# Optimization experiments

Measured on AMD Instinct MI355X. Metric: run time of the kernel, lower is better.

Reference implementation:

```python
import jax, jax.numpy as jnp
from jax import lax
import numpy as np

VOCAB, EMB = 50000, 50
B, S = 256, 2048
K1, K2 = 8, 4  # k-max pool sizes (k1=8 hardcoded, top_k=4)


def conv1d_valid(x, w, b):
    # x: [B, L, Cin], w: [KW, Cin, Cout] (TF conv1d layout), VALID padding
    return lax.conv_general_dilated(
        x, w, window_strides=(1,), padding='VALID',
        dimension_numbers=('NWC', 'WIO', 'NWC')) + b


def kmax_pool(signal, k):
    # Dynamic k-max pooling: select k positions with largest channel-mean
    # excitement (tf.nn.top_k sorted=False + gather over axis 1).
    excitements = jnp.mean(signal, axis=2)            # [B, L]
    _, idx = lax.top_k(excitements, k)                # [B, k]
    return jnp.take_along_axis(signal, idx[:, :, None], axis=1)  # [B, k, C]


def setup_inputs() -> dict:
    key = jax.random.key(0)
    ks = jax.random.split(key, 6)
    x = jax.random.randint(ks[0], (B, S), 0, VOCAB, dtype=jnp.int32)
    embeddings = jax.random.normal(ks[1], (VOCAB, EMB), jnp.float32)
    W1 = jax.random.normal(ks[2], (7, EMB, 6), jnp.float32) * 0.05
    b1 = jnp.zeros((6,), jnp.float32)
    W2 = jax.random.normal(ks[3], (5, 6, 14), jnp.float32) * 0.1
    b2 = jnp.zeros((14,), jnp.float32)
    Wd = jax.random.normal(ks[4], (14, 1), jnp.float32) * 0.1
    bd = jnp.zeros((1,), jnp.float32)
    return {"x": x, "embeddings": embeddings, "W1": W1, "b1": b1,
            "W2": W2, "b2": b2, "Wd": Wd, "bd": bd}


def reference(x, embeddings, W1, b1, W2, b2, Wd, bd):
    signal = embeddings[x]                                  # [B, S, 50]
    signal = jnp.pad(signal, ((0, 0), (6, 6), (0, 0)))      # [B, S+12, 50]
    signal = conv1d_valid(signal, W1, b1)                   # [B, S+6, 6]
    signal = kmax_pool(signal, K1)                          # [B, 8, 6]
    signal = jax.nn.sigmoid(signal)
    signal = jnp.pad(signal, ((0, 0), (4, 4), (0, 0)))      # [B, 16, 6]
    signal = conv1d_valid(signal, W2, b2)                   # [B, 12, 14]
    signal = kmax_pool(signal, K2)                          # [B, 4, 14]
    signal = jnp.mean(signal, axis=1)                       # [B, 14]
    dense = signal @ Wd + bd                                # [B, 1]
    output = jnp.mean(dense)                                # scalar
    return jax.nn.sigmoid(output)
```

## Files before the change

kernel.cpp:

```cpp
#include <hip/hip_runtime.h>
#include <math.h>

#define SEQ   2048
#define VOCAB 50000
#define EMBD  50
#define L1OUT 2054
#define NTOK  2060
#define DSTR  2064

__global__ void __launch_bounds__(384)
prep_kernel(const float* __restrict__ W1, float* __restrict__ ws) {
    int t = threadIdx.x;
    if (t < 350) {
        float s = 0.f;
        #pragma unroll
        for (int c = 0; c < 6; ++c) s += W1[t * 6 + c];
        ws[t] = s * (1.0f / 6.0f);
    } else if (t < 352) {
        ws[t] = 0.f;
    }
}

__global__ void __launch_bounds__(256)
build_d(const float* __restrict__ emb, const float* __restrict__ wm,
        float* __restrict__ D) {
    int v = blockIdx.x * 256 + threadIdx.x;
    if (v >= VOCAB) return;
    const float2* row = (const float2*)(emb + (size_t)v * EMBD);
    float d[7] = {0.f, 0.f, 0.f, 0.f, 0.f, 0.f, 0.f};
    for (int e = 0; e < 25; ++e) {
        float2 r = row[e];
        #pragma unroll
        for (int kw = 0; kw < 7; ++kw)
            d[kw] = fmaf(r.y, wm[kw * 50 + 2 * e + 1],
                    fmaf(r.x, wm[kw * 50 + 2 * e], d[kw]));
    }
    float4* out = (float4*)(D + (size_t)v * 8);
    out[0] = make_float4(d[0], d[1], d[2], d[3]);
    out[1] = make_float4(d[4], d[5], d[6], 0.f);
}

template<int USE_D>
__global__ void __launch_bounds__(512, 1)
dcnn_main(const int* __restrict__ x, const float* __restrict__ emb,
          const float* __restrict__ W1, const float* __restrict__ b1,
          const float* __restrict__ W2, const float* __restrict__ b2,
          const float* __restrict__ Wd, const float* __restrict__ bd,
          const float* __restrict__ Dtab, const float* __restrict__ wm,
          float* __restrict__ dense_out)
{
    __shared__ float Dv[7][DSTR];
    __shared__ float exc[L1OUT];
    __shared__ float blv[8];
    __shared__ int   bli[8];
    __shared__ int   topi[8];
    __shared__ float part[240];
    __shared__ float s1p[16][6];
    __shared__ float out2[12][14];
    __shared__ float exc2[12];

    const int b   = blockIdx.x;
    const int tid = threadIdx.x;
    const int* xb = x + b * SEQ;

    for (int i = tid; i < NTOK; i += 512) {
        int g = i - 6;
        float d0 = 0.f, d1 = 0.f, d2 = 0.f, d3 = 0.f,
              d4 = 0.f, d5 = 0.f, d6 = 0.f;
        if (g >= 0 && g < SEQ) {
            int tok = xb[g];
            if (USE_D) {
                const float4* dp = (const float4*)(Dtab + (size_t)tok * 8);
                float4 lo = dp[0], hi = dp[1];
                d0 = lo.x; d1 = lo.y; d2 = lo.z; d3 = lo.w;
                d4 = hi.x; d5 = hi.y; d6 = hi.z;
            } else {
                const float2* row = (const float2*)(emb + (size_t)tok * EMBD);
                float dd[7] = {0.f, 0.f, 0.f, 0.f, 0.f, 0.f, 0.f};
                for (int e = 0; e < 25; ++e) {
                    float2 r = row[e];
                    #pragma unroll
                    for (int kw = 0; kw < 7; ++kw)
                        dd[kw] = fmaf(r.y, wm[kw * 50 + 2 * e + 1],
                                 fmaf(r.x, wm[kw * 50 + 2 * e], dd[kw]));
                }
                d0 = dd[0]; d1 = dd[1]; d2 = dd[2]; d3 = dd[3];
                d4 = dd[4]; d5 = dd[5]; d6 = dd[6];
            }
        }
        Dv[0][i] = d0; Dv[1][i] = d1; Dv[2][i] = d2; Dv[3][i] = d3;
        Dv[4][i] = d4; Dv[5][i] = d5; Dv[6][i] = d6;
    }
    __syncthreads();

    for (int t = tid; t < L1OUT; t += 512) {
        float s = ((Dv[0][t] + Dv[1][t + 1]) + (Dv[2][t + 2] + Dv[3][t + 3]))
                + ((Dv[4][t + 4] + Dv[5][t + 5]) + Dv[6][t + 6]);
        exc[t] = s;
    }
    __syncthreads();

    #pragma unroll 1
    for (int r = 0; r < 8; ++r) {
        float bv = -INFINITY; int bi = L1OUT;
        for (int t = tid; t < L1OUT; t += 512) {
            float v = exc[t];
            if (v > bv || (v == bv && t < bi)) { bv = v; bi = t; }
        }
        #pragma unroll
        for (int off = 32; off > 0; off >>= 1) {
            float ov = __shfl_down(bv, off, 64);
            int   oi = __shfl_down(bi, off, 64);
            if (ov > bv || (ov == bv && oi < bi)) { bv = ov; bi = oi; }
        }
        if ((tid & 63) == 0) { blv[tid >> 6] = bv; bli[tid >> 6] = bi; }
        __syncthreads();
        if (tid == 0) {
            #pragma unroll
            for (int w = 1; w < 8; ++w) {
                float ov = blv[w]; int oi = bli[w];
                if (ov > bv || (ov == bv && oi < bi)) { bv = ov; bi = oi; }
            }
            topi[r] = bi;
            exc[bi] = -INFINITY;
        }
        __syncthreads();
    }

    if (tid < 96) ((float*)s1p)[tid] = 0.f;
    if (tid < 240) {
        int r = tid / 30, sub = tid - r * 30;
        int c = sub / 5,  eq  = sub - c * 5;
        int t = topi[r];
        float acc = 0.f;
        for (int kw = 0; kw < 7; ++kw) {
            int g = t + kw - 6;
            if (g >= 0 && g < SEQ) {
                const float* row = emb + (size_t)xb[g] * EMBD + eq * 10;
                const float* wp  = W1 + (kw * 50 + eq * 10) * 6 + c;
                #pragma unroll
                for (int e = 0; e < 10; ++e)
                    acc = fmaf(row[e], wp[e * 6], acc);
            }
        }
        part[tid] = acc;
    }
    __syncthreads();
    if (tid < 48) {
        int r = tid / 6, c = tid - r * 6;
        float s = b1[c];
        #pragma unroll
        for (int eq = 0; eq < 5; ++eq) s += part[r * 30 + c * 5 + eq];
        s1p[4 + r][c] = 1.0f / (1.0f + expf(-s));
    }
    __syncthreads();

    if (tid < 168) {
        int t = tid / 14, c = tid - t * 14;
        float acc = b2[c];
        #pragma unroll
        for (int kw = 0; kw < 5; ++kw)
            #pragma unroll
            for (int i = 0; i < 6; ++i)
                acc = fmaf(s1p[t + kw][i], W2[(kw * 6 + i) * 14 + c], acc);
        out2[t][c] = acc;
    }
    __syncthreads();
    if (tid < 12) {
        float s = 0.f;
        #pragma unroll
        for (int c = 0; c < 14; ++c) s += out2[tid][c];
        exc2[tid] = s / 14.0f;
    }
    __syncthreads();

    if (tid == 0) {
        float ev[12];
        #pragma unroll
        for (int t = 0; t < 12; ++t) ev[t] = exc2[t];
        int sel[4];
        #pragma unroll 1
        for (int r = 0; r < 4; ++r) {
            float bv = -INFINITY; int bi = 0;
            for (int t = 0; t < 12; ++t)
                if (ev[t] > bv) { bv = ev[t]; bi = t; }
            sel[r] = bi; ev[bi] = -INFINITY;
        }
        float dense = bd[0];
        #pragma unroll
        for (int c = 0; c < 14; ++c) {
            float pool = 0.25f * ((out2[sel[0]][c] + out2[sel[1]][c]) +
                                  (out2[sel[2]][c] + out2[sel[3]][c]));
            dense = fmaf(pool, Wd[c], dense);
        }
        dense_out[b] = dense;
    }
}

__global__ void __launch_bounds__(256)
finalize_kernel(const float* __restrict__ dense, float* __restrict__ out) {
    int tid = threadIdx.x;
    float v = dense[tid];
    #pragma unroll
    for (int off = 32; off > 0; off >>= 1) v += __shfl_down(v, off, 64);
    __shared__ float ws4[4];
    if ((tid & 63) == 0) ws4[tid >> 6] = v;
    __syncthreads();
    if (tid == 0) {
        float s = (ws4[0] + ws4[1]) + (ws4[2] + ws4[3]);
        float m = s * (1.0f / 256.0f);
        out[0] = 1.0f / (1.0f + expf(-m));
    }
}

extern "C" void kernel_launch(void* const* d_in, const int* in_sizes, int n_in,
                              void* d_out, int out_size, void* d_ws, size_t ws_size,
                              hipStream_t stream) {
    const int*   x   = (const int*)d_in[0];
    const float* emb = (const float*)d_in[1];
    const float* W1  = (const float*)d_in[2];
    const float* b1  = (const float*)d_in[3];
    const float* W2  = (const float*)d_in[4];
    const float* b2  = (const float*)d_in[5];
    const float* Wd  = (const float*)d_in[6];
    const float* bd  = (const float*)d_in[7];
    float* ws = (float*)d_ws;

    const size_t needD = (size_t)(384 + VOCAB * 8 + 256) * sizeof(float);

    prep_kernel<<<1, 384, 0, stream>>>(W1, ws);
    if (ws_size >= needD) {
        float* D     = ws + 384;
        float* dense = ws + 384 + VOCAB * 8;
        build_d<<<(VOCAB + 255) / 256, 256, 0, stream>>>(emb, ws, D);
        dcnn_main<1><<<256, 512, 0, stream>>>(x, emb, W1, b1, W2, b2, Wd, bd,
                                              D, ws, dense);
        finalize_kernel<<<1, 256, 0, stream>>>(dense, (float*)d_out);
    } else {
        float* dense = ws + 352;
        dcnn_main<0><<<256, 512, 0, stream>>>(x, emb, W1, b1, W2, b2, Wd, bd,
                                              ws, ws, dense);
        finalize_kernel<<<1, 256, 0, stream>>>(dense, (float*)d_out);
    }
}
```

Measured before the change: 107.6 us.

## Fuse prep and finalize into neighbours, register-resident two-level top-k selection

The weight-mean prep is folded into build_d, with each block recomputing it into shared memory. The finalize kernel is replaced by an atomic accumulate plus a last-block-done counter inside dcnn_main, which cuts two launches. The 8-round block-wide top-k, which needed two barriers per round over a shared array, becomes per-wave register top-8 selection followed by a single-wave merge of 64 candidates. The costs are redundant weight-mean work in every build_d block and a float atomicAdd whose summation order is nondeterministic.

```diff
diff --git a/kernel.cpp b/kernel.cpp
--- a/kernel.cpp
+++ b/kernel.cpp
@@ -16,15 +16,26 @@
         #pragma unroll
         for (int c = 0; c < 6; ++c) s += W1[t * 6 + c];
         ws[t] = s * (1.0f / 6.0f);
-    } else if (t < 352) {
+    } else if (t < 354) {
         ws[t] = 0.f;
     }
 }
 
 __global__ void __launch_bounds__(256)
-build_d(const float* __restrict__ emb, const float* __restrict__ wm,
-        float* __restrict__ D) {
-    int v = blockIdx.x * 256 + threadIdx.x;
+build_d(const float* __restrict__ emb, const float* __restrict__ W1,
+        float* __restrict__ D, float* __restrict__ acc, int* __restrict__ cnt) {
+    __shared__ float wm[352];
+    int t = threadIdx.x;
+    for (int i = t; i < 350; i += 256) {
+        float s = 0.f;
+        #pragma unroll
+        for (int c = 0; c < 6; ++c) s += W1[i * 6 + c];
+        wm[i] = s * (1.0f / 6.0f);
+    }
+    if (blockIdx.x == 0 && t == 0) { *acc = 0.f; *cnt = 0; }
+    __syncthreads();
+
+    int v = blockIdx.x * 256 + t;
     if (v >= VOCAB) return;
     const float2* row = (const float2*)(emb + (size_t)v * EMBD);
     float d[7] = {0.f, 0.f, 0.f, 0.f, 0.f, 0.f, 0.f};
@@ -47,12 +58,12 @@
           const float* __restrict__ W2, const float* __restrict__ b2,
           const float* __restrict__ Wd, const float* __restrict__ bd,
           const float* __restrict__ Dtab, const float* __restrict__ wm,
-          float* __restrict__ dense_out)
+          float* __restrict__ acc, int* __restrict__ cnt,
+          float* __restrict__ out)
 {
     __shared__ float Dv[7][DSTR];
-    __shared__ float exc[L1OUT];
-    __shared__ float blv[8];
-    __shared__ int   bli[8];
+    __shared__ float cand_v[64];
+    __shared__ int   cand_i[64];
     __shared__ int   topi[8];
     __shared__ float part[240];
     __shared__ float s1p[16][6];
@@ -93,46 +104,68 @@
     }
     __syncthreads();
 
-    for (int t = tid; t < L1OUT; t += 512) {
-        float s = ((Dv[0][t] + Dv[1][t + 1]) + (Dv[2][t + 2] + Dv[3][t + 3]))
-                + ((Dv[4][t + 4] + Dv[5][t + 5]) + Dv[6][t + 6]);
-        exc[t] = s;
-    }
-    __syncthreads();
-
+    float ev[5];
+    #pragma unroll
+    for (int k = 0; k < 4; ++k) {
+        int t = tid + 512 * k;
+        ev[k] = ((Dv[0][t] + Dv[1][t + 1]) + (Dv[2][t + 2] + Dv[3][t + 3]))
+              + ((Dv[4][t + 4] + Dv[5][t + 5]) + Dv[6][t + 6]);
+    }
+    if (tid < 6) {
+        int t = tid + 2048;
+        ev[4] = ((Dv[0][t] + Dv[1][t + 1]) + (Dv[2][t + 2] + Dv[3][t + 3]))
+              + ((Dv[4][t + 4] + Dv[5][t + 5]) + Dv[6][t + 6]);
+    } else {
+        ev[4] = -INFINITY;
+    }
+
+    const int wid  = tid >> 6;
+    const int lane = tid & 63;
     #pragma unroll 1
     for (int r = 0; r < 8; ++r) {
-        float bv = -INFINITY; int bi = L1OUT;
-        for (int t = tid; t < L1OUT; t += 512) {
-            float v = exc[t];
-            if (v > bv || (v == bv && t < bi)) { bv = v; bi = t; }
-        }
-        #pragma unroll
-        for (int off = 32; off > 0; off >>= 1) {
-            float ov = __shfl_down(bv, off, 64);
-            int   oi = __shfl_down(bi, off, 64);
+        float bv = ev[0]; int bk = 0;
+        #pragma unroll
+        for (int k = 1; k < 5; ++k)
+            if (ev[k] > bv) { bv = ev[k]; bk = k; }
+        int bi = tid + 512 * bk;
+        #pragma unroll
+        for (int off = 1; off < 64; off <<= 1) {
+            float ov = __shfl_xor(bv, off, 64);
+            int   oi = __shfl_xor(bi, off, 64);
             if (ov > bv || (ov == bv && oi < bi)) { bv = ov; bi = oi; }
         }
-        if ((tid & 63) == 0) { blv[tid >> 6] = bv; bli[tid >> 6] = bi; }
-        __syncthreads();
-        if (tid == 0) {
+        #pragma unroll
+        for (int k = 0; k < 5; ++k)
+            if (tid + 512 * k == bi) ev[k] = -INFINITY;
+        if (lane == 0) { cand_v[wid * 8 + r] = bv; cand_i[wid * 8 + r] = bi; }
+    }
+    __syncthreads();
+
+    if (tid < 64) {
+        float cv = cand_v[tid];
+        int   ci = cand_i[tid];
+        #pragma unroll 1
+        for (int r = 0; r < 8; ++r) {
+            float bv = cv; int bi = ci;
             #pragma unroll
-            for (int w = 1; w < 8; ++w) {
-                float ov = blv[w]; int oi = bli[w];
+            for (int off = 1; off < 64; off <<= 1) {
+                float ov = __shfl_xor(bv, off, 64);
+                int   oi = __shfl_xor(bi, off, 64);
                 if (ov > bv || (ov == bv && oi < bi)) { bv = ov; bi = oi; }
             }
-            topi[r] = bi;
-            exc[bi] = -INFINITY;
-        }
-        __syncthreads();
-    }
+            if (cv == bv && ci == bi) cv = -INFINITY;
+            if (tid == 0) topi[r] = bi;
+        }
+    }
+    __syncthreads();
 
     if (tid < 96) ((float*)s1p)[tid] = 0.f;
     if (tid < 240) {
         int r = tid / 30, sub = tid - r * 30;
         int c = sub / 5,  eq  = sub - c * 5;
         int t = topi[r];
-        float acc = 0.f;
+        float a2 = 0.f;
+        #pragma unroll
         for (int kw = 0; kw < 7; ++kw) {
             int g = t + kw - 6;
             if (g >= 0 && g < SEQ) {
@@ -140,10 +173,10 @@
                 const float* wp  = W1 + (kw * 50 + eq * 10) * 6 + c;
                 #pragma unroll
                 for (int e = 0; e < 10; ++e)
-                    acc = fmaf(row[e], wp[e * 6], acc);
+                    a2 = fmaf(row[e], wp[e * 6], a2);
             }
         }
-        part[tid] = acc;
+        part[tid] = a2;
     }
     __syncthreads();
     if (tid < 48) {
@@ -157,13 +190,13 @@
 
     if (tid < 168) {
         int t = tid / 14, c = tid - t * 14;
-        float acc = b2[c];
+        float a2 = b2[c];
         #pragma unroll
         for (int kw = 0; kw < 5; ++kw)
             #pragma unroll
             for (int i = 0; i < 6; ++i)
-                acc = fmaf(s1p[t + kw][i], W2[(kw * 6 + i) * 14 + c], acc);
-        out2[t][c] = acc;
+                a2 = fmaf(s1p[t + kw][i], W2[(kw * 6 + i) * 14 + c], a2);
+        out2[t][c] = a2;
     }
     __syncthreads();
     if (tid < 12) {
@@ -175,16 +208,17 @@
     __syncthreads();
 
     if (tid == 0) {
-        float ev[12];
-        #pragma unroll
-        for (int t = 0; t < 12; ++t) ev[t] = exc2[t];
+        float evl[12];
+        #pragma unroll
+        for (int t = 0; t < 12; ++t) evl[t] = exc2[t];
         int sel[4];
         #pragma unroll 1
         for (int r = 0; r < 4; ++r) {
             float bv = -INFINITY; int bi = 0;
+            #pragma unroll
             for (int t = 0; t < 12; ++t)
-                if (ev[t] > bv) { bv = ev[t]; bi = t; }
-            sel[r] = bi; ev[bi] = -INFINITY;
+                if (evl[t] > bv) { bv = evl[t]; bi = t; }
+            sel[r] = bi; evl[bi] = -INFINITY;
         }
         float dense = bd[0];
         #pragma unroll
@@ -193,23 +227,14 @@
                                   (out2[sel[2]][c] + out2[sel[3]][c]));
             dense = fmaf(pool, Wd[c], dense);
         }
-        dense_out[b] = dense;
-    }
-}
-
-__global__ void __launch_bounds__(256)
-finalize_kernel(const float* __restrict__ dense, float* __restrict__ out) {
-    int tid = threadIdx.x;
-    float v = dense[tid];
-    #pragma unroll
-    for (int off = 32; off > 0; off >>= 1) v += __shfl_down(v, off, 64);
-    __shared__ float ws4[4];
-    if ((tid & 63) == 0) ws4[tid >> 6] = v;
-    __syncthreads();
-    if (tid == 0) {
-        float s = (ws4[0] + ws4[1]) + (ws4[2] + ws4[3]);
-        float m = s * (1.0f / 256.0f);
-        out[0] = 1.0f / (1.0f + expf(-m));
+        atomicAdd(acc, dense);
+        __threadfence();
+        int done = atomicAdd(cnt, 1);
+        if (done == 255) {
+            __threadfence();
+            float s = atomicAdd(acc, 0.0f);
+            out[0] = 1.0f / (1.0f + expf(-s * (1.0f / 256.0f)));
+        }
     }
 }
 
@@ -226,20 +251,20 @@
     const float* bd  = (const float*)d_in[7];
     float* ws = (float*)d_ws;
 
-    const size_t needD = (size_t)(384 + VOCAB * 8 + 256) * sizeof(float);
-
-    prep_kernel<<<1, 384, 0, stream>>>(W1, ws);
+    const size_t needD = (size_t)(384 + VOCAB * 8 + 8) * sizeof(float);
+
     if (ws_size >= needD) {
-        float* D     = ws + 384;
-        float* dense = ws + 384 + VOCAB * 8;
-        build_d<<<(VOCAB + 255) / 256, 256, 0, stream>>>(emb, ws, D);
+        float* D   = ws + 384;
+        float* acc = D + VOCAB * 8;
+        int*   cnt = (int*)(acc + 1);
+        build_d<<<(VOCAB + 255) / 256, 256, 0, stream>>>(emb, W1, D, acc, cnt);
         dcnn_main<1><<<256, 512, 0, stream>>>(x, emb, W1, b1, W2, b2, Wd, bd,
-                                              D, ws, dense);
-        finalize_kernel<<<1, 256, 0, stream>>>(dense, (float*)d_out);
+                                              D, ws, acc, cnt, (float*)d_out);
     } else {
-        float* dense = ws + 352;
+        float* acc = ws + 352;
+        int*   cnt = (int*)(ws + 353);
+        prep_kernel<<<1, 384, 0, stream>>>(W1, ws);
         dcnn_main<0><<<256, 512, 0, stream>>>(x, emb, W1, b1, W2, b2, Wd, bd,
-                                              ws, ws, dense);
-        finalize_kernel<<<1, 256, 0, stream>>>(dense, (float*)d_out);
-    }
-}
+                                              ws, ws, acc, cnt, (float*)d_out);
+    }
+}
```

Measured after the change: 108.0 us. No clear change (+0.3%).
